# Kernel tuning notes

Measured on AMD Instinct MI355X. Metric: run time of the kernel, lower is better.

Reference implementation:

```python
import jax, jax.numpy as jnp
import numpy as np

N_QUBITS = 12
FAST_DEPTH = 4
FAST_DECAY = 0.9
LATENT = 512
BATCH = 2048


def _apply_ry(state, theta, wire):
    # state: (B, 2**n) real; RY is a real rotation. PennyLane default.qubit:
    # wire 0 is the most-significant bit of the state index.
    B = state.shape[0]
    s = state.reshape(B, 1 << wire, 2, -1)
    h = theta * 0.5
    c = jnp.cos(h)[:, None, None]
    sn = jnp.sin(h)[:, None, None]
    s0, s1 = s[:, :, 0], s[:, :, 1]
    out = jnp.stack([c * s0 - sn * s1, sn * s0 + c * s1], axis=2)
    return out.reshape(state.shape)


def _apply_cnot_adjacent(state, wire):
    # CNOT with control=wire, target=wire+1 (nearest-neighbor chain)
    B = state.shape[0]
    s = state.reshape(B, 1 << wire, 2, 2, -1)
    out = jnp.stack([s[:, :, 0], s[:, :, 1, ::-1]], axis=2)
    return out.reshape(state.shape)


def _fwp_circuit(x, fast, n_qubits, n_outputs):
    # x: (B, n_qubits) RY encoding angles; fast: (B, depth, n_qubits)
    B = x.shape[0]
    dim = 1 << n_qubits
    # Hadamard layer on |0...0> -> uniform positive real amplitudes.
    state = jnp.full((B, dim), 2.0 ** (-n_qubits / 2), dtype=x.dtype)
    for w in range(n_qubits):
        state = _apply_ry(state, x[:, w], w)
    for layer in range(fast.shape[1]):
        for w in range(n_qubits - 1):
            state = _apply_cnot_adjacent(state, w)
        for w in range(n_qubits):
            state = _apply_ry(state, fast[:, layer, w], w)
    probs = state * state  # real state -> |amp|^2
    outs = []
    for w in range(n_outputs):
        p = probs.reshape(B, 1 << w, 2, -1)
        outs.append(p[:, :, 0].sum(axis=(1, 2)) - p[:, :, 1].sum(axis=(1, 2)))
    return jnp.stack(outs, axis=1)  # (B, n_outputs) PauliZ expvals


def setup_inputs() -> dict:
    key = jax.random.key(0)
    ks = jax.random.split(key, 6)
    n, depth, latent = N_QUBITS, FAST_DEPTH, LATENT
    return {
        "x_t": jax.random.normal(ks[0], (BATCH, n), jnp.float32),
        "fast_prev": jax.random.normal(ks[1], (BATCH, depth, n), jnp.float32) * 0.1,
        "W_enc": jax.random.normal(ks[2], (latent, n), jnp.float32) / np.sqrt(n).astype(np.float32),
        "b_enc": jnp.zeros((latent,), jnp.float32),
        "W_upd": jax.random.normal(ks[3], (depth * n, latent), jnp.float32) / np.sqrt(latent).astype(np.float32),
        "b_upd": jnp.zeros((depth * n,), jnp.float32),
        "W_ro": jax.random.normal(ks[4], (1, n), jnp.float32) / np.sqrt(n).astype(np.float32),
        "b_ro": jnp.zeros((1,), jnp.float32),
    }


def reference(x_t, fast_prev, W_enc, b_enc, W_upd, b_upd, W_ro, b_ro):
    latent = jnp.tanh(x_t @ W_enc.T + b_enc)
    delta = (latent @ W_upd.T + b_upd).reshape(x_t.shape[0], FAST_DEPTH, N_QUBITS)
    fast_next = FAST_DECAY * fast_prev + delta
    q_out = _fwp_circuit(x_t, fast_next, N_QUBITS, N_QUBITS)  # n_outputs = n_qubits
    y_t = q_out @ W_ro.T + b_ro
    return (y_t, fast_next)
```

## Files before the change

kernel.cpp:

```cpp
#include <hip/hip_runtime.h>

static constexpr int NQ    = 12;
static constexpr int DEPTH = 4;
static constexpr int LAT   = 512;
static constexpr int FAST  = DEPTH * NQ;
static constexpr float DECAY = 0.9f;


__device__ __forceinline__ float i2f(int x) { return __int_as_float(x); }

template<int M>
__device__ __forceinline__ float xpartner(float x, int lane) {
    int xi = __float_as_int(x);
    if constexpr (M == 1) {
        return i2f(__builtin_amdgcn_update_dpp(xi, xi, 0xB1, 0xF, 0xF, true));
    } else if constexpr (M == 2) {
        return i2f(__builtin_amdgcn_update_dpp(xi, xi, 0x4E, 0xF, 0xF, true));
    } else if constexpr (M == 4) {
        int t = __builtin_amdgcn_update_dpp(xi, xi, 0x141, 0xF, 0xF, true);
        return i2f(__builtin_amdgcn_update_dpp(t, t, 0x1B, 0xF, 0xF, true));
    } else if constexpr (M == 8) {
        return i2f(__builtin_amdgcn_update_dpp(xi, xi, 0x128, 0xF, 0xF, true));
    } else if constexpr (M == 16) {
#if __has_builtin(__builtin_amdgcn_permlane16_swap)
        auto r = __builtin_amdgcn_permlane16_swap((unsigned)xi, (unsigned)xi, false, false);
        return i2f((int)(r[0] ^ r[1]) ^ xi);
#else
        return __shfl_xor(x, 16, 64);
#endif
    } else {
#if __has_builtin(__builtin_amdgcn_permlane32_swap)
        auto r = __builtin_amdgcn_permlane32_swap((unsigned)xi, (unsigned)xi, false, false);
        return i2f((int)(r[0] ^ r[1]) ^ xi);
#else
        return __shfl_xor(x, 32, 64);
#endif
    }
}

template<int W>
__device__ __forceinline__ void ry_lane(float (&v)[64], int lane, float c, float s) {
    constexpr int M = 1 << (5 - W);
    float t = (lane & M) ? s : -s;
    #pragma unroll
    for (int r = 0; r < 64; r++) {
        float p = xpartner<M>(v[r], lane);
        v[r] = c * v[r] + t * p;
    }
}

template<int W>
__device__ __forceinline__ void ry_reg(float (&v)[64], float c, float s) {
    constexpr int S = 1 << (11 - W);
    #pragma unroll
    for (int r0 = 0; r0 < 64; r0++) {
        if ((r0 & S) == 0) {
            float a = v[r0];
            float b = v[r0 + S];
            v[r0]     = c * a - s * b;
            v[r0 + S] = s * a + c * b;
        }
    }
}

template<int W>
__device__ __forceinline__ void apply_cnot_reg(float (&v)[64]) {
    constexpr int CBS = 1 << (11 - W);
    constexpr int TBS = 1 << (10 - W);
    #pragma unroll
    for (int r = 0; r < 64; r++) {
        if ((r & CBS) != 0 && (r & TBS) == 0) {
            float tmp = v[r];
            v[r]       = v[r | TBS];
            v[r | TBS] = tmp;
        }
    }
}

template<int W>
__device__ __forceinline__ void cnot_reg_chain(float (&v)[64]) {
    if constexpr (W < 11) {
        apply_cnot_reg<W>(v);
        cnot_reg_chain<W + 1>(v);
    }
}

template<int W>
__device__ __forceinline__ void layer_rys(float (&v)[64], int lane, const float* ang) {
    if constexpr (W < 12) {
        float h = 0.5f * ang[W];
        float c = __cosf(h), s = __sinf(h);
        if constexpr (W < 6) ry_lane<W>(v, lane, c, s);
        else                 ry_reg<W>(v, c, s);
        layer_rys<W + 1>(v, lane, ang);
    }
}

__global__ __launch_bounds__(256, 2)
void fwp_kernel(const float* __restrict__ x_t,
                const float* __restrict__ fast_prev,
                const float* __restrict__ W_enc,
                const float* __restrict__ b_enc,
                const float* __restrict__ W_upd,
                const float* __restrict__ b_upd,
                const float* __restrict__ W_ro,
                const float* __restrict__ b_ro,
                float* __restrict__ out_y,
                float* __restrict__ out_fast) {
    const int lane = threadIdx.x & 63;
    const int wv   = threadIdx.x >> 6;
    const int b    = blockIdx.x * 4 + wv;

    __shared__ float s_lat[4][LAT];
    __shared__ float s_ang[4][FAST];

    float xr = (lane < NQ) ? x_t[b * NQ + lane] : 0.0f;
    float xa[NQ];
    #pragma unroll
    for (int k = 0; k < NQ; k++) xa[k] = __shfl(xr, k, 64);

    #pragma unroll
    for (int t = 0; t < LAT / 64; t++) {
        int j = lane + 64 * t;
        const float4* wr = (const float4*)(W_enc + j * NQ);
        float4 a0 = wr[0], a1 = wr[1], a2 = wr[2];
        float sum = b_enc[j]
            + a0.x * xa[0] + a0.y * xa[1] + a0.z * xa[2]  + a0.w * xa[3]
            + a1.x * xa[4] + a1.y * xa[5] + a1.z * xa[6]  + a1.w * xa[7]
            + a2.x * xa[8] + a2.y * xa[9] + a2.z * xa[10] + a2.w * xa[11];
        s_lat[wv][j] = tanhf(sum);
    }
    __syncthreads();

    if (lane < FAST) {
        const float4* wr = (const float4*)(W_upd + lane * LAT);
        const float4* lr = (const float4*)(s_lat[wv]);
        float sum = b_upd[lane];
        #pragma unroll 16
        for (int j = 0; j < LAT / 4; j++) {
            float4 w4 = wr[j];
            float4 l4 = lr[j];
            sum += w4.x * l4.x + w4.y * l4.y + w4.z * l4.z + w4.w * l4.w;
        }
        float ang = DECAY * fast_prev[b * FAST + lane] + sum;
        s_ang[wv][lane] = ang;
        out_fast[b * FAST + lane] = ang;
    }
    __syncthreads();

    float g0[NQ], g1[NQ];
    #pragma unroll
    for (int w = 0; w < NQ; w++) {
        float h = 0.5f * xa[w];
        float c = __cosf(h), s = __sinf(h);
        g0[w] = (c - s) * 0.70710678118654752f;
        g1[w] = (c + s) * 0.70710678118654752f;
    }
    float L = 1.0f;
    #pragma unroll
    for (int w = 0; w < 6; w++)
        L *= ((lane >> (5 - w)) & 1) ? g1[w] : g0[w];

    float v[64];
    v[0] = L;
    #pragma unroll
    for (int w = 6; w < NQ; w++) {
        const int S = 1 << (11 - w);
        #pragma unroll
        for (int r = 0; r < 64; r += 2 * S) {
            v[r + S] = v[r] * g1[w];
            v[r]     = v[r] * g0[w];
        }
    }

    int csrc = lane;
    #pragma unroll
    for (int w = 4; w >= 0; w--)
        csrc ^= ((csrc >> (5 - w)) & 1) << (4 - w);
    const int csrc4 = csrc << 2;

    #pragma unroll 1
    for (int layer = 0; layer < DEPTH; layer++) {
        #pragma unroll
        for (int r = 0; r < 64; r++)
            v[r] = i2f(__builtin_amdgcn_ds_bpermute(csrc4, __float_as_int(v[r])));
        bool c5 = (lane & 1) != 0;
        #pragma unroll
        for (int r0 = 0; r0 < 32; r0++) {
            float a = v[r0], bb = v[r0 + 32];
            v[r0]      = c5 ? bb : a;
            v[r0 + 32] = c5 ? a : bb;
        }
        cnot_reg_chain<6>(v);
        layer_rys<0>(v, lane, &s_ang[wv][layer * NQ]);
    }

    float tot = 0.0f, pw[6] = {0, 0, 0, 0, 0, 0};
    #pragma unroll
    for (int r = 0; r < 64; r++) {
        float p = v[r] * v[r];
        tot += p;
        pw[0] += (r & 32) ? -p : p;
        pw[1] += (r & 16) ? -p : p;
        pw[2] += (r & 8)  ? -p : p;
        pw[3] += (r & 4)  ? -p : p;
        pw[4] += (r & 2)  ? -p : p;
        pw[5] += (r & 1)  ? -p : p;
    }
    float sl = 0.0f;
    #pragma unroll
    for (int w = 0; w < 6; w++) {
        float c = W_ro[w];
        sl += ((lane >> (5 - w)) & 1) ? -c : c;
    }
    float y = sl * tot;
    #pragma unroll
    for (int k = 0; k < 6; k++) y += W_ro[6 + k] * pw[k];
    #pragma unroll
    for (int m = 32; m >= 1; m >>= 1) y += __shfl_xor(y, m, 64);
    if (lane == 0) out_y[b] = y + b_ro[0];
}

extern "C" void kernel_launch(void* const* d_in, const int* in_sizes, int n_in,
                              void* d_out, int out_size, void* d_ws, size_t ws_size,
                              hipStream_t stream) {
    const float* x_t       = (const float*)d_in[0];
    const float* fast_prev = (const float*)d_in[1];
    const float* W_enc     = (const float*)d_in[2];
    const float* b_enc     = (const float*)d_in[3];
    const float* W_upd     = (const float*)d_in[4];
    const float* b_upd     = (const float*)d_in[5];
    const float* W_ro      = (const float*)d_in[6];
    const float* b_ro      = (const float*)d_in[7];
    float* out = (float*)d_out;

    fwp_kernel<<<2048 / 4, 256, 0, stream>>>(x_t, fast_prev, W_enc, b_enc,
                                             W_upd, b_upd, W_ro, b_ro,
                                             out , out + 2048 );
}
```

Before: 126.3 us.

## Split each sample's state vector across two wavefronts with LDS exchange

Each batch sample is now handled by two 64-lane wavefronts in a 128-thread block instead of one wavefront, so each thread holds 32 amplitudes instead of 64. The top qubit is mapped to the wavefront index, and its RY rotation is done through an LDS exchange bracketed by __syncthreads. The W_upd dot product is split across the two waves and reduced in shared memory. The aim is lower register pressure and higher occupancy, paid for with block-level barriers, extra LDS traffic (16KB per block) and twice as many blocks.

```diff
diff --git a/kernel.cpp b/kernel.cpp
--- a/kernel.cpp
+++ b/kernel.cpp
@@ -39,21 +39,21 @@
 }
 
 template<int W>
-__device__ __forceinline__ void ry_lane(float (&v)[64], int lane, float c, float s) {
-    constexpr int M = 1 << (5 - W);
+__device__ __forceinline__ void ry_lane(float (&v)[32], int lane, float c, float s) {
+    constexpr int M = 1 << (6 - W);
     float t = (lane & M) ? s : -s;
     #pragma unroll
-    for (int r = 0; r < 64; r++) {
+    for (int r = 0; r < 32; r++) {
         float p = xpartner<M>(v[r], lane);
         v[r] = c * v[r] + t * p;
     }
 }
 
 template<int W>
-__device__ __forceinline__ void ry_reg(float (&v)[64], float c, float s) {
+__device__ __forceinline__ void ry_reg(float (&v)[32], float c, float s) {
     constexpr int S = 1 << (11 - W);
     #pragma unroll
-    for (int r0 = 0; r0 < 64; r0++) {
+    for (int r0 = 0; r0 < 32; r0++) {
         if ((r0 & S) == 0) {
             float a = v[r0];
             float b = v[r0 + S];
@@ -64,11 +64,11 @@
 }
 
 template<int W>
-__device__ __forceinline__ void apply_cnot_reg(float (&v)[64]) {
+__device__ __forceinline__ void apply_cnot_reg(float (&v)[32]) {
     constexpr int CBS = 1 << (11 - W);
     constexpr int TBS = 1 << (10 - W);
     #pragma unroll
-    for (int r = 0; r < 64; r++) {
+    for (int r = 0; r < 32; r++) {
         if ((r & CBS) != 0 && (r & TBS) == 0) {
             float tmp = v[r];
             v[r]       = v[r | TBS];
@@ -78,7 +78,7 @@
 }
 
 template<int W>
-__device__ __forceinline__ void cnot_reg_chain(float (&v)[64]) {
+__device__ __forceinline__ void cnot_reg_chain(float (&v)[32]) {
     if constexpr (W < 11) {
         apply_cnot_reg<W>(v);
         cnot_reg_chain<W + 1>(v);
@@ -86,17 +86,17 @@
 }
 
 template<int W>
-__device__ __forceinline__ void layer_rys(float (&v)[64], int lane, const float* ang) {
+__device__ __forceinline__ void layer_rys(float (&v)[32], int lane, const float* ang) {
     if constexpr (W < 12) {
-        float h = 0.5f * ang[W];
-        float c = __cosf(h), s = __sinf(h);
-        if constexpr (W < 6) ry_lane<W>(v, lane, c, s);
-        else                 ry_reg<W>(v, c, s);
+        float hh = 0.5f * ang[W];
+        float c = __cosf(hh), s = __sinf(hh);
+        if constexpr (W <= 6) ry_lane<W>(v, lane, c, s);
+        else                  ry_reg<W>(v, c, s);
         layer_rys<W + 1>(v, lane, ang);
     }
 }
 
-__global__ __launch_bounds__(256, 2)
+__global__ __launch_bounds__(128, 4)
 void fwp_kernel(const float* __restrict__ x_t,
                 const float* __restrict__ fast_prev,
                 const float* __restrict__ W_enc,
@@ -107,12 +107,16 @@
                 const float* __restrict__ b_ro,
                 float* __restrict__ out_y,
                 float* __restrict__ out_fast) {
-    const int lane = threadIdx.x & 63;
-    const int wv   = threadIdx.x >> 6;
-    const int b    = blockIdx.x * 4 + wv;
-
-    __shared__ float s_lat[4][LAT];
-    __shared__ float s_ang[4][FAST];
+    const int tid  = threadIdx.x;
+    const int lane = tid & 63;
+    const int h    = tid >> 6;
+    const int b    = blockIdx.x;
+
+    __shared__ float s_xch[2 * 2048];
+    __shared__ float s_lat[LAT];
+    __shared__ float s_ang[FAST];
+    __shared__ float s_red[FAST][2];
+    __shared__ float s_y[2];
 
     float xr = (lane < NQ) ? x_t[b * NQ + lane] : 0.0f;
     float xa[NQ];
@@ -120,105 +124,125 @@
     for (int k = 0; k < NQ; k++) xa[k] = __shfl(xr, k, 64);
 
     #pragma unroll
-    for (int t = 0; t < LAT / 64; t++) {
-        int j = lane + 64 * t;
+    for (int t = 0; t < LAT / 128; t++) {
+        int j = tid + 128 * t;
         const float4* wr = (const float4*)(W_enc + j * NQ);
         float4 a0 = wr[0], a1 = wr[1], a2 = wr[2];
         float sum = b_enc[j]
             + a0.x * xa[0] + a0.y * xa[1] + a0.z * xa[2]  + a0.w * xa[3]
             + a1.x * xa[4] + a1.y * xa[5] + a1.z * xa[6]  + a1.w * xa[7]
             + a2.x * xa[8] + a2.y * xa[9] + a2.z * xa[10] + a2.w * xa[11];
-        s_lat[wv][j] = tanhf(sum);
+        s_lat[j] = tanhf(sum);
     }
     __syncthreads();
 
     if (lane < FAST) {
-        const float4* wr = (const float4*)(W_upd + lane * LAT);
-        const float4* lr = (const float4*)(s_lat[wv]);
-        float sum = b_upd[lane];
+        const float4* wr = (const float4*)(W_upd + lane * LAT + h * (LAT / 2));
+        const float4* lr = (const float4*)(s_lat + h * (LAT / 2));
+        float sum = 0.0f;
         #pragma unroll 16
-        for (int j = 0; j < LAT / 4; j++) {
+        for (int j = 0; j < LAT / 8; j++) {
             float4 w4 = wr[j];
             float4 l4 = lr[j];
             sum += w4.x * l4.x + w4.y * l4.y + w4.z * l4.z + w4.w * l4.w;
         }
-        float ang = DECAY * fast_prev[b * FAST + lane] + sum;
-        s_ang[wv][lane] = ang;
-        out_fast[b * FAST + lane] = ang;
+        s_red[lane][h] = sum;
+    }
+    __syncthreads();
+    if (tid < FAST) {
+        float ang = DECAY * fast_prev[b * FAST + tid]
+                  + s_red[tid][0] + s_red[tid][1] + b_upd[tid];
+        s_ang[tid] = ang;
+        out_fast[b * FAST + tid] = ang;
     }
     __syncthreads();
 
     float g0[NQ], g1[NQ];
     #pragma unroll
     for (int w = 0; w < NQ; w++) {
-        float h = 0.5f * xa[w];
-        float c = __cosf(h), s = __sinf(h);
+        float hh = 0.5f * xa[w];
+        float c = __cosf(hh), s = __sinf(hh);
         g0[w] = (c - s) * 0.70710678118654752f;
         g1[w] = (c + s) * 0.70710678118654752f;
     }
-    float L = 1.0f;
-    #pragma unroll
-    for (int w = 0; w < 6; w++)
-        L *= ((lane >> (5 - w)) & 1) ? g1[w] : g0[w];
-
-    float v[64];
+    float L = h ? g1[0] : g0[0];
+    #pragma unroll
+    for (int w = 1; w <= 6; w++)
+        L *= ((lane >> (6 - w)) & 1) ? g1[w] : g0[w];
+
+    float v[32];
     v[0] = L;
     #pragma unroll
-    for (int w = 6; w < NQ; w++) {
+    for (int w = 7; w < NQ; w++) {
         const int S = 1 << (11 - w);
         #pragma unroll
-        for (int r = 0; r < 64; r += 2 * S) {
+        for (int r = 0; r < 32; r += 2 * S) {
             v[r + S] = v[r] * g1[w];
             v[r]     = v[r] * g0[w];
         }
     }
 
-    int csrc = lane;
-    #pragma unroll
-    for (int w = 4; w >= 0; w--)
-        csrc ^= ((csrc >> (5 - w)) & 1) << (4 - w);
+    const int csrc  = ((lane ^ (lane >> 1)) & 31) | ((((lane >> 5) & 1) ^ h) << 5);
     const int csrc4 = csrc << 2;
 
     #pragma unroll 1
     for (int layer = 0; layer < DEPTH; layer++) {
+        const float* ang = &s_ang[layer * NQ];
         #pragma unroll
-        for (int r = 0; r < 64; r++)
+        for (int r = 0; r < 32; r++)
             v[r] = i2f(__builtin_amdgcn_ds_bpermute(csrc4, __float_as_int(v[r])));
-        bool c5 = (lane & 1) != 0;
+        bool cc = (lane & 1) != 0;
         #pragma unroll
-        for (int r0 = 0; r0 < 32; r0++) {
-            float a = v[r0], bb = v[r0 + 32];
-            v[r0]      = c5 ? bb : a;
-            v[r0 + 32] = c5 ? a : bb;
-        }
-        cnot_reg_chain<6>(v);
-        layer_rys<0>(v, lane, &s_ang[wv][layer * NQ]);
-    }
-
-    float tot = 0.0f, pw[6] = {0, 0, 0, 0, 0, 0};
-    #pragma unroll
-    for (int r = 0; r < 64; r++) {
+        for (int r0 = 0; r0 < 16; r0++) {
+            float a = v[r0], bb = v[r0 + 16];
+            v[r0]      = cc ? bb : a;
+            v[r0 + 16] = cc ? a : bb;
+        }
+        cnot_reg_chain<7>(v);
+
+        {
+            float hh = 0.5f * ang[0];
+            float c = __cosf(hh), s = __sinf(hh);
+            __syncthreads();
+            #pragma unroll
+            for (int r = 0; r < 32; r++)
+                s_xch[h * 2048 + r * 64 + lane] = v[r];
+            __syncthreads();
+            float t = h ? s : -s;
+            #pragma unroll
+            for (int r = 0; r < 32; r++) {
+                float p = s_xch[(1 - h) * 2048 + r * 64 + lane];
+                v[r] = c * v[r] + t * p;
+            }
+        }
+        layer_rys<1>(v, lane, ang);
+    }
+
+    float tot = 0.0f, pw[5] = {0, 0, 0, 0, 0};
+    #pragma unroll
+    for (int r = 0; r < 32; r++) {
         float p = v[r] * v[r];
         tot += p;
-        pw[0] += (r & 32) ? -p : p;
-        pw[1] += (r & 16) ? -p : p;
-        pw[2] += (r & 8)  ? -p : p;
-        pw[3] += (r & 4)  ? -p : p;
-        pw[4] += (r & 2)  ? -p : p;
-        pw[5] += (r & 1)  ? -p : p;
-    }
-    float sl = 0.0f;
-    #pragma unroll
-    for (int w = 0; w < 6; w++) {
+        pw[0] += (r & 16) ? -p : p;
+        pw[1] += (r & 8)  ? -p : p;
+        pw[2] += (r & 4)  ? -p : p;
+        pw[3] += (r & 2)  ? -p : p;
+        pw[4] += (r & 1)  ? -p : p;
+    }
+    float sl = h ? -W_ro[0] : W_ro[0];
+    #pragma unroll
+    for (int w = 1; w <= 6; w++) {
         float c = W_ro[w];
-        sl += ((lane >> (5 - w)) & 1) ? -c : c;
+        sl += ((lane >> (6 - w)) & 1) ? -c : c;
     }
     float y = sl * tot;
     #pragma unroll
-    for (int k = 0; k < 6; k++) y += W_ro[6 + k] * pw[k];
+    for (int k = 0; k < 5; k++) y += W_ro[7 + k] * pw[k];
     #pragma unroll
     for (int m = 32; m >= 1; m >>= 1) y += __shfl_xor(y, m, 64);
-    if (lane == 0) out_y[b] = y + b_ro[0];
+    if (lane == 0) s_y[h] = y;
+    __syncthreads();
+    if (tid == 0) out_y[b] = s_y[0] + s_y[1] + b_ro[0];
 }
 
 extern "C" void kernel_launch(void* const* d_in, const int* in_sizes, int n_in,
@@ -234,7 +258,7 @@
     const float* b_ro      = (const float*)d_in[7];
     float* out = (float*)d_out;
 
-    fwp_kernel<<<2048 / 4, 256, 0, stream>>>(x_t, fast_prev, W_enc, b_enc,
-                                             W_upd, b_upd, W_ro, b_ro,
-                                             out , out + 2048 );
-}
+    fwp_kernel<<<2048, 128, 0, stream>>>(x_t, fast_prev, W_enc, b_enc,
+                                         W_upd, b_upd, W_ro, b_ro,
+                                         out , out + 2048 );
+}
```

Result: slower. 132.9 us (+5.2%).
